# Performance work log

Hardware: AMD Instinct MI355X
Metric: run time of the kernel (lower is better)

Reference implementation:

```python
import jax, jax.numpy as jnp
import numpy as np

N, B, D = 8, 4096, 1024
LOG_2PI = np.float32(np.log(2.0 * np.pi))


def setup_inputs() -> dict:
    key = jax.random.key(0)
    k1, k2 = jax.random.split(key)
    means = jax.random.normal(k1, (N, B, D), dtype=jnp.float32)
    logsigmas = jax.random.normal(k2, (N, B, D), dtype=jnp.float32)
    return {"means": means, "logsigmas": logsigmas}


def reference(means, logsigmas):
    # Sequential product of diagonal Gaussians.
    # Original builds DxD diag matrices + MVN log_prob; mathematically this is
    # purely elementwise over D plus a sum for the log-normalizer.
    m0, lv0 = means[0], logsigmas[0]
    lz0 = jnp.zeros(means.shape[1], dtype=means.dtype)

    def step(carry, inp):
        m1, lv1, lz = carry          # prior mean, log-variance, accumulated log_z
        m2, lv2 = inp                # next component
        v1 = jnp.exp(lv1)
        v2 = jnp.exp(lv2)
        iv1 = 1.0 / v1
        iv2 = 1.0 / v2
        cvar = 1.0 / (iv1 + iv2)              # combined variance (diag of C)
        cmean = cvar * (m1 * iv1 + m2 * iv2)  # combined mean
        s = v1 + v2 + 1e-6                    # covariance of the normalizer Gaussian
        # MVN(m2, diag(s)).log_prob(m1) == sum of univariate normal log-pdfs
        log_z = -0.5 * jnp.sum((m1 - m2) ** 2 / s + jnp.log(s) + LOG_2PI, axis=-1)
        return (cmean, jnp.log(cvar), lz + log_z), None

    (post_mean, post_logvar, log_z_total), _ = jax.lax.scan(
        step, (m0, lv0, lz0), (means[1:], logsigmas[1:])
    )
    return post_mean, post_logvar, log_z_total
```

## Files before the change

kernel.cpp:

```cpp
#include <hip/hip_runtime.h>
#include <math.h>

#define NN 8
#define BB 4096
#define DD 1024
#define LOG_2PI 1.8378770664093453f


#define GLOAD_LDS16(g, l)                                                  \
    __builtin_amdgcn_global_load_lds(                                      \
        (const __attribute__((address_space(1))) unsigned int*)(g),        \
        (__attribute__((address_space(3))) unsigned int*)(l), 16, 0, 0)

__global__ __launch_bounds__(256) void mpc_kernel(
    const float* __restrict__ means,
    const float* __restrict__ logsig,
    float* __restrict__ out_mean,
    float* __restrict__ out_logvar,
    float* __restrict__ out_logz)
{
    __shared__ float smem[16 * DD];

    const int b = blockIdx.x;
    const int t = threadIdx.x;
    const int wave = t >> 6;
    const size_t rowoff = (size_t)b * DD + (size_t)t * 4;
    const size_t plane = (size_t)BB * DD;

#pragma unroll
    for (int n = 0; n < NN; ++n) {
        const float* gm = means  + (size_t)n * plane + rowoff;
        const float* gl = logsig + (size_t)n * plane + rowoff;
        float* lm = &smem[n * DD + wave * 256];
        float* ll = &smem[(NN + n) * DD + wave * 256];
        GLOAD_LDS16(gm, lm);
        GLOAD_LDS16(gl, ll);
    }
    __syncthreads();

    float m1[4], v1[4], iv1[4];
    {
        float4 mm = *(const float4*)&smem[0 * DD + t * 4];
        float4 ll = *(const float4*)&smem[NN * DD + t * 4];
        float m[4] = {mm.x, mm.y, mm.z, mm.w};
        float l[4] = {ll.x, ll.y, ll.z, ll.w};
#pragma unroll
        for (int j = 0; j < 4; ++j) {
            m1[j]  = m[j];
            v1[j]  = __expf(l[j]);
            iv1[j] = __expf(-l[j]);
        }
    }

    float z = 0.0f;

#pragma unroll
    for (int n = 1; n < NN; ++n) {
        float4 mm = *(const float4*)&smem[n * DD + t * 4];
        float4 ll = *(const float4*)&smem[(NN + n) * DD + t * 4];
        float m2[4] = {mm.x, mm.y, mm.z, mm.w};
        float l2[4] = {ll.x, ll.y, ll.z, ll.w};
#pragma unroll
        for (int j = 0; j < 4; ++j) {
            float v2  = __expf(l2[j]);
            float iv2 = __expf(-l2[j]);
            float s   = v1[j] + v2 + 1e-6f;
            float diff = m1[j] - m2[j];
            z += diff * diff * __builtin_amdgcn_rcpf(s) + __logf(s);
            float iv_new = iv1[j] + iv2;
            float cvar   = __builtin_amdgcn_rcpf(iv_new);
            m1[j]  = cvar * (m1[j] * iv1[j] + m2[j] * iv2);
            v1[j]  = cvar;
            iv1[j] = iv_new;
        }
    }

    float4 om = make_float4(m1[0], m1[1], m1[2], m1[3]);
    float4 ol = make_float4(__logf(v1[0]), __logf(v1[1]),
                            __logf(v1[2]), __logf(v1[3]));
    *(float4*)(out_mean + rowoff)   = om;
    *(float4*)(out_logvar + rowoff) = ol;

#pragma unroll
    for (int o = 32; o > 0; o >>= 1)
        z += __shfl_down(z, o, 64);

    __shared__ float sz[4];
    const int lane = t & 63;
    if (lane == 0) sz[wave] = z;
    __syncthreads();
    if (t == 0) {
        float total = sz[0] + sz[1] + sz[2] + sz[3];
        out_logz[b] = -0.5f * (total + (float)((NN - 1) * DD) * LOG_2PI);
    }
}

extern "C" void kernel_launch(void* const* d_in, const int* in_sizes, int n_in,
                              void* d_out, int out_size, void* d_ws, size_t ws_size,
                              hipStream_t stream) {
    const float* means  = (const float*)d_in[0];
    const float* logsig = (const float*)d_in[1];
    float* out = (float*)d_out;
    float* out_mean   = out;
    float* out_logvar = out + (size_t)BB * DD;
    float* out_logz   = out + 2 * (size_t)BB * DD;
    mpc_kernel<<<BB, 256, 0, stream>>>(means, logsig, out_mean, out_logvar, out_logz);
}
```

Before: 283.6 us.

## Persistent single-wave blocks with double-buffered async LDS prefetch over chunks

Replaces one 256-thread block per row with 1280 persistent 64-thread blocks that walk 256-element chunks. Each block prefetches the next chunk into a second LDS buffer while computing the current one, synchronising with explicit vmcnt waits instead of barriers. The per-row log-normalizer becomes four atomic partial sums, which needs a memset before launch. It also rotates plane load order per block to spread memory traffic. The cost is atomics, an extra memset launch, and reliance on hand-tuned vmcnt counts, which must match the number of outstanding loads and stores.

```diff
diff --git a/kernel.cpp b/kernel.cpp
--- a/kernel.cpp
+++ b/kernel.cpp
@@ -4,6 +4,9 @@
 #define NN 8
 #define BB 4096
 #define DD 1024
+#define CHUNK 256
+#define NCHUNK (BB * 4)
+#define NBLK 1280
 #define LOG_2PI 1.8378770664093453f
 
 
@@ -12,86 +15,105 @@
         (const __attribute__((address_space(1))) unsigned int*)(g),        \
         (__attribute__((address_space(3))) unsigned int*)(l), 16, 0, 0)
 
-__global__ __launch_bounds__(256) void mpc_kernel(
+#define WAITVM(imm) asm volatile("s_waitcnt vmcnt(" #imm ")" ::: "memory")
+
+__global__ __launch_bounds__(64) void mpc_kernel(
     const float* __restrict__ means,
     const float* __restrict__ logsig,
     float* __restrict__ out_mean,
     float* __restrict__ out_logvar,
     float* __restrict__ out_logz)
 {
-    __shared__ float smem[16 * DD];
+    __shared__ float smem[2][16 * CHUNK];
 
-    const int b = blockIdx.x;
-    const int t = threadIdx.x;
-    const int wave = t >> 6;
-    const size_t rowoff = (size_t)b * DD + (size_t)t * 4;
+    const int lane = threadIdx.x;
+    const int rot  = blockIdx.x & 7;
     const size_t plane = (size_t)BB * DD;
 
+    auto stage = [&](int ch, int s) {
+        const size_t base = (size_t)(ch >> 2) * DD
+                          + (size_t)(ch & 3) * CHUNK + (size_t)lane * 4;
 #pragma unroll
-    for (int n = 0; n < NN; ++n) {
-        const float* gm = means  + (size_t)n * plane + rowoff;
-        const float* gl = logsig + (size_t)n * plane + rowoff;
-        float* lm = &smem[n * DD + wave * 256];
-        float* ll = &smem[(NN + n) * DD + wave * 256];
-        GLOAD_LDS16(gm, lm);
-        GLOAD_LDS16(gl, ll);
-    }
-    __syncthreads();
+        for (int i = 0; i < NN; ++i) {
+            const int n = (i + rot) & 7;
+            GLOAD_LDS16(means  + (size_t)n * plane + base,
+                        &smem[s][(2 * n + 0) * CHUNK]);
+            GLOAD_LDS16(logsig + (size_t)n * plane + base,
+                        &smem[s][(2 * n + 1) * CHUNK]);
+        }
+    };
 
-    float m1[4], v1[4], iv1[4];
-    {
-        float4 mm = *(const float4*)&smem[0 * DD + t * 4];
-        float4 ll = *(const float4*)&smem[NN * DD + t * 4];
-        float m[4] = {mm.x, mm.y, mm.z, mm.w};
-        float l[4] = {ll.x, ll.y, ll.z, ll.w};
+    auto work = [&](int ch, int s) {
+        const int b = ch >> 2;
+        const size_t base = (size_t)b * DD
+                          + (size_t)(ch & 3) * CHUNK + (size_t)lane * 4;
+        const float* buf = smem[s];
+
+        float m1[4], v1[4], iv1[4];
+        {
+            float4 mm = *(const float4*)&buf[0 * CHUNK + lane * 4];
+            float4 ll = *(const float4*)&buf[1 * CHUNK + lane * 4];
+            float m[4] = {mm.x, mm.y, mm.z, mm.w};
+            float l[4] = {ll.x, ll.y, ll.z, ll.w};
 #pragma unroll
-        for (int j = 0; j < 4; ++j) {
-            m1[j]  = m[j];
-            v1[j]  = __expf(l[j]);
-            iv1[j] = __expf(-l[j]);
+            for (int j = 0; j < 4; ++j) {
+                m1[j]  = m[j];
+                v1[j]  = __expf(l[j]);
+                iv1[j] = __expf(-l[j]);
+            }
         }
-    }
+        float z = 0.0f;
+#pragma unroll
+        for (int n = 1; n < NN; ++n) {
+            float4 mm = *(const float4*)&buf[(2 * n + 0) * CHUNK + lane * 4];
+            float4 ll = *(const float4*)&buf[(2 * n + 1) * CHUNK + lane * 4];
+            float m2[4] = {mm.x, mm.y, mm.z, mm.w};
+            float l2[4] = {ll.x, ll.y, ll.z, ll.w};
+#pragma unroll
+            for (int j = 0; j < 4; ++j) {
+                float v2  = __expf(l2[j]);
+                float iv2 = __expf(-l2[j]);
+                float s2  = v1[j] + v2 + 1e-6f;
+                float diff = m1[j] - m2[j];
+                z += diff * diff * __builtin_amdgcn_rcpf(s2) + __logf(s2);
+                float iv_new = iv1[j] + iv2;
+                float cvar   = __builtin_amdgcn_rcpf(iv_new);
+                m1[j]  = cvar * (m1[j] * iv1[j] + m2[j] * iv2);
+                v1[j]  = cvar;
+                iv1[j] = iv_new;
+            }
+        }
+        float4 om = make_float4(m1[0], m1[1], m1[2], m1[3]);
+        float4 ol = make_float4(__logf(v1[0]), __logf(v1[1]),
+                                __logf(v1[2]), __logf(v1[3]));
+        *(float4*)(out_mean + base)   = om;
+        *(float4*)(out_logvar + base) = ol;
+#pragma unroll
+        for (int o = 32; o > 0; o >>= 1)
+            z += __shfl_down(z, o, 64);
+        if (lane == 0) {
+            float partial = -0.5f * z
+                          - 0.125f * (float)((NN - 1) * DD) * LOG_2PI;
+            atomicAdd(out_logz + b, partial);
+        }
+    };
 
-    float z = 0.0f;
-
-#pragma unroll
-    for (int n = 1; n < NN; ++n) {
-        float4 mm = *(const float4*)&smem[n * DD + t * 4];
-        float4 ll = *(const float4*)&smem[(NN + n) * DD + t * 4];
-        float m2[4] = {mm.x, mm.y, mm.z, mm.w};
-        float l2[4] = {ll.x, ll.y, ll.z, ll.w};
-#pragma unroll
-        for (int j = 0; j < 4; ++j) {
-            float v2  = __expf(l2[j]);
-            float iv2 = __expf(-l2[j]);
-            float s   = v1[j] + v2 + 1e-6f;
-            float diff = m1[j] - m2[j];
-            z += diff * diff * __builtin_amdgcn_rcpf(s) + __logf(s);
-            float iv_new = iv1[j] + iv2;
-            float cvar   = __builtin_amdgcn_rcpf(iv_new);
-            m1[j]  = cvar * (m1[j] * iv1[j] + m2[j] * iv2);
-            v1[j]  = cvar;
-            iv1[j] = iv_new;
+    int ch = blockIdx.x;
+    int s  = 0;
+    stage(ch, 0);
+    while (true) {
+        const int nxt = ch + NBLK;
+        if (nxt < NCHUNK) {
+            stage(nxt, s ^ 1);
+            WAITVM(16);
+            work(ch, s);
+            ch = nxt;
+            s ^= 1;
+        } else {
+            WAITVM(3);
+            work(ch, s);
+            break;
         }
-    }
-
-    float4 om = make_float4(m1[0], m1[1], m1[2], m1[3]);
-    float4 ol = make_float4(__logf(v1[0]), __logf(v1[1]),
-                            __logf(v1[2]), __logf(v1[3]));
-    *(float4*)(out_mean + rowoff)   = om;
-    *(float4*)(out_logvar + rowoff) = ol;
-
-#pragma unroll
-    for (int o = 32; o > 0; o >>= 1)
-        z += __shfl_down(z, o, 64);
-
-    __shared__ float sz[4];
-    const int lane = t & 63;
-    if (lane == 0) sz[wave] = z;
-    __syncthreads();
-    if (t == 0) {
-        float total = sz[0] + sz[1] + sz[2] + sz[3];
-        out_logz[b] = -0.5f * (total + (float)((NN - 1) * DD) * LOG_2PI);
     }
 }
 
@@ -104,5 +126,6 @@
     float* out_mean   = out;
     float* out_logvar = out + (size_t)BB * DD;
     float* out_logz   = out + 2 * (size_t)BB * DD;
-    mpc_kernel<<<BB, 256, 0, stream>>>(means, logsig, out_mean, out_logvar, out_logz);
+    hipMemsetAsync(out_logz, 0, BB * sizeof(float), stream);
+    mpc_kernel<<<NBLK, 64, 0, stream>>>(means, logsig, out_mean, out_logvar, out_logz);
 }
```

New measurement: 321.5 us. 13.4% more time.
